# Kernel optimization log

Hardware: AMD Instinct MI355X
Metric: run time of the kernel (lower is better)

The kernel has to match this reference:

```python
import jax, jax.numpy as jnp
import numpy as np

C = 64
DQK = C // 8  # query/key channels


def setup_inputs() -> dict:
    key = jax.random.key(0)
    ks = jax.random.split(key, 8)
    B, H, W = 4, 64, 64
    x = jax.random.normal(ks[0], (B, C, H, W), dtype=jnp.float32)
    # 1x1 conv weights stored as (out_ch, in_ch); biases as (out_ch,)
    wq = jax.random.normal(ks[1], (DQK, C), dtype=jnp.float32) * 0.05
    bq = jnp.zeros((DQK,), dtype=jnp.float32)
    wk = jax.random.normal(ks[2], (DQK, C), dtype=jnp.float32) * 0.05
    bk = jnp.zeros((DQK,), dtype=jnp.float32)
    wv = jax.random.normal(ks[3], (C, C), dtype=jnp.float32) * 0.05
    bv = jnp.zeros((C,), dtype=jnp.float32)
    gamma = jnp.zeros((1,), dtype=jnp.float32)
    return {"x": x, "wq": wq, "bq": bq, "wk": wk, "bk": bk,
            "wv": wv, "bv": bv, "gamma": gamma}


def reference(x, wq, bq, wk, bk, wv, bv, gamma):
    B, Cc, H, W = x.shape
    N = H * W
    xf = x.reshape(B, Cc, N)  # (B, C, N)
    # 1x1 convs == channel-wise matmuls
    q = jnp.einsum('oc,bcn->bon', wq, xf) + bq[None, :, None]  # (B, dqk, N)
    k = jnp.einsum('oc,bcn->bon', wk, xf) + bk[None, :, None]  # (B, dqk, N)
    v = jnp.einsum('oc,bcn->bon', wv, xf) + bv[None, :, None]  # (B, C, N)
    # qk = q^T k -> (B, N, N), softmax over last dim
    qk = jnp.einsum('bdn,bdm->bnm', q, k)
    attn = jax.nn.softmax(qk, axis=-1)
    # out = v @ attn^T : out[b,c,i] = sum_j v[b,c,j] * attn[b,i,j]
    out = jnp.einsum('bcj,bij->bci', v, attn)
    out = out.reshape(B, Cc, H, W)
    return gamma * out + x
```

## Files before the change

kernel.cpp:

```cpp
#include <hip/hip_runtime.h>
#include <cmath>

namespace {

constexpr int B = 4;
constexpr int C = 64;
constexpr int N = 4096;
constexpr float LOG2E = 1.4426950408889634f;

typedef __bf16 bf16x8 __attribute__((ext_vector_type(8)));
typedef float f32x16 __attribute__((ext_vector_type(16)));
typedef unsigned short u16;

union B8 {
  int4 i;
  bf16x8 h;
  unsigned int w[4];
};

__device__ inline u16 f2bf(float f) {
  unsigned int u = __float_as_uint(f);
  u += 0x7FFFu + ((u >> 16) & 1u);
  return (u16)(u >> 16);
}

__device__ inline unsigned int cvt_pk_bf16(float lo, float hi) {
  unsigned int r;
  asm("v_cvt_pk_bf16_f32 %0, %1, %2" : "=v"(r) : "v"(lo), "v"(hi));
  return r;
}

__device__ inline float exp2_fast(float x) {
#if __has_builtin(__builtin_amdgcn_exp2f)
  return __builtin_amdgcn_exp2f(x);
#else
  return exp2f(x);
#endif
}

__device__ inline void pl32_swap(unsigned int& a, unsigned int& b) {
#if __has_builtin(__builtin_amdgcn_permlane32_swap)
  auto r = __builtin_amdgcn_permlane32_swap(a, b, false, false);
  a = (unsigned int)r[0];
  b = (unsigned int)r[1];
#else
  asm volatile("s_nop 1\n\tv_permlane32_swap_b32 %0, %1" : "+v"(a), "+v"(b));
#endif
}

__global__ __launch_bounds__(256) void qkv_kernel(
    const float* __restrict__ x,
    const float* __restrict__ wq, const float* __restrict__ bq,
    const float* __restrict__ wk, const float* __restrict__ bk,
    const float* __restrict__ wv, const float* __restrict__ bv,
    u16* __restrict__ qt, u16* __restrict__ kt, u16* __restrict__ vo) {
  const int bid = blockIdx.x;
  const int cg = bid & 3;
  const int nt = (bid >> 2) & 63;
  const int b = bid >> 8;
  const int t = threadIdx.x;
  const int nn = t & 63;
  const int wid = __builtin_amdgcn_readfirstlane(t >> 6);
  const int n = nt * 64 + nn;
  const float* xb = x + (size_t)b * C * N + n;

  const int c0 = cg * 16 + wid * 4;
  float a0 = bv[c0], a1 = bv[c0 + 1], a2 = bv[c0 + 2], a3 = bv[c0 + 3];

  if (cg == 0) {
    const int o0 = wid * 2;
    float qa0 = bq[o0], qa1 = bq[o0 + 1];
    float ka0 = bk[o0], ka1 = bk[o0 + 1];
    #pragma unroll 8
    for (int c = 0; c < C; ++c) {
      const float xv = xb[(size_t)c * N];
      a0 = fmaf(wv[(c0 + 0) * C + c], xv, a0);
      a1 = fmaf(wv[(c0 + 1) * C + c], xv, a1);
      a2 = fmaf(wv[(c0 + 2) * C + c], xv, a2);
      a3 = fmaf(wv[(c0 + 3) * C + c], xv, a3);
      qa0 = fmaf(wq[o0 * C + c], xv, qa0);
      qa1 = fmaf(wq[(o0 + 1) * C + c], xv, qa1);
      ka0 = fmaf(wk[o0 * C + c], xv, ka0);
      ka1 = fmaf(wk[(o0 + 1) * C + c], xv, ka1);
    }
    const unsigned int qw =
        (unsigned int)f2bf(qa0 * LOG2E) | ((unsigned int)f2bf(qa1 * LOG2E) << 16);
    const unsigned int kw =
        (unsigned int)f2bf(ka0) | ((unsigned int)f2bf(ka1) << 16);
    *reinterpret_cast<unsigned int*>(qt + ((size_t)b * N + n) * 8 + o0) = qw;
    *reinterpret_cast<unsigned int*>(kt + ((size_t)b * N + n) * 8 + o0) = kw;
  } else {
    #pragma unroll 8
    for (int c = 0; c < C; ++c) {
      const float xv = xb[(size_t)c * N];
      a0 = fmaf(wv[(c0 + 0) * C + c], xv, a0);
      a1 = fmaf(wv[(c0 + 1) * C + c], xv, a1);
      a2 = fmaf(wv[(c0 + 2) * C + c], xv, a2);
      a3 = fmaf(wv[(c0 + 3) * C + c], xv, a3);
    }
  }

  const size_t tb = ((size_t)b * (N / 16) + (n >> 4)) * (C * 16) + (n & 15);
  vo[tb + (size_t)(c0 + 0) * 16] = f2bf(a0);
  vo[tb + (size_t)(c0 + 1) * 16] = f2bf(a1);
  vo[tb + (size_t)(c0 + 2) * 16] = f2bf(a2);
  vo[tb + (size_t)(c0 + 3) * 16] = f2bf(a3);
}

__global__ __launch_bounds__(512, 1) void attn_kernel(
    const u16* __restrict__ qt, const u16* __restrict__ kt,
    const u16* __restrict__ vv, const float* __restrict__ x,
    const float* __restrict__ gamma, float* __restrict__ out) {
  const int b = blockIdx.x >> 6;
  const int i0 = (blockIdx.x & 63) * 64;
  const int t = threadIdx.x;
  const int lane = t & 63;
  const int w = __builtin_amdgcn_readfirstlane(t >> 6);
  const int il = lane & 31;
  const int hi = lane >> 5;

  __shared__ float l_lds[8][32];
  __shared__ u16 o_lds[8][32][66];

  B8 qf0, qf1;
  if (hi == 0) {
    qf0.i = *reinterpret_cast<const int4*>(qt + ((size_t)b * N + i0 + il) * 8);
    qf1.i = *reinterpret_cast<const int4*>(qt + ((size_t)b * N + i0 + 32 + il) * 8);
  } else {
    qf0.i = make_int4(0, 0, 0, 0);
    qf1.i = make_int4(0, 0, 0, 0);
  }

  const u16* ktb = kt + (size_t)b * N * 8;
  const u16* vbase = vv + (size_t)b * (N / 16) * (C * 16) + il * 16 + hi * 8;

  f32x16 accA0, accB0, accA1, accB1, zero16;
  #pragma unroll
  for (int r = 0; r < 16; ++r) {
    accA0[r] = 0.f; accB0[r] = 0.f; accA1[r] = 0.f; accB1[r] = 0.f;
    zero16[r] = 0.f;
  }
  float lrun0 = 0.f, lrun1 = 0.f;

  B8 kfA, va0A, va1A, vb0A, vb1A;
  B8 kfB, va0B, va1B, vb0B, vb1B;

  auto LOAD = [&](int jt, B8& kf, B8& va0, B8& va1, B8& vb0, B8& vb1) {
    const int j0 = w * 512 + jt * 32;
    if (hi == 0)
      kf.i = *reinterpret_cast<const int4*>(ktb + (size_t)(j0 + il) * 8);
    else
      kf.i = make_int4(0, 0, 0, 0);
    const u16* vp = vbase + (size_t)(j0 >> 4) * (C * 16);
    va0.i = *reinterpret_cast<const int4*>(vp);
    va1.i = *reinterpret_cast<const int4*>(vp + 1024);
    vb0.i = *reinterpret_cast<const int4*>(vp + 512);
    vb1.i = *reinterpret_cast<const int4*>(vp + 1536);
  };

  auto SMPACK = [&](const f32x16& S, float& lrun, B8& pf0, B8& pf1) {
    float p[16];
    #pragma unroll
    for (int r = 0; r < 16; ++r) p[r] = exp2_fast(S[r]);
    const float t0 = (p[0] + p[1]) + (p[2] + p[3]);
    const float t1 = (p[4] + p[5]) + (p[6] + p[7]);
    const float t2 = (p[8] + p[9]) + (p[10] + p[11]);
    const float t3 = (p[12] + p[13]) + (p[14] + p[15]);
    lrun += (t0 + t1) + (t2 + t3);
    unsigned a0 = cvt_pk_bf16(p[0], p[1]);
    unsigned a1 = cvt_pk_bf16(p[2], p[3]);
    unsigned b0 = cvt_pk_bf16(p[4], p[5]);
    unsigned b1 = cvt_pk_bf16(p[6], p[7]);
    pl32_swap(a0, b0);
    pl32_swap(a1, b1);
    pf0.w[0] = a0; pf0.w[1] = a1; pf0.w[2] = b0; pf0.w[3] = b1;
    a0 = cvt_pk_bf16(p[8], p[9]);
    a1 = cvt_pk_bf16(p[10], p[11]);
    b0 = cvt_pk_bf16(p[12], p[13]);
    b1 = cvt_pk_bf16(p[14], p[15]);
    pl32_swap(a0, b0);
    pl32_swap(a1, b1);
    pf1.w[0] = a0; pf1.w[1] = a1; pf1.w[2] = b0; pf1.w[3] = b1;
  };

  auto COMPUTE = [&](const B8& kf, const B8& va0, const B8& va1, const B8& vb0,
                     const B8& vb1) {
    f32x16 S0 = __builtin_amdgcn_mfma_f32_32x32x16_bf16(kf.h, qf0.h, zero16, 0, 0, 0);
    f32x16 S1 = __builtin_amdgcn_mfma_f32_32x32x16_bf16(kf.h, qf1.h, zero16, 0, 0, 0);
    B8 p00, p01, p10, p11;
    SMPACK(S0, lrun0, p00, p01);
    SMPACK(S1, lrun1, p10, p11);
    accA0 = __builtin_amdgcn_mfma_f32_32x32x16_bf16(va0.h, p00.h, accA0, 0, 0, 0);
    accA0 = __builtin_amdgcn_mfma_f32_32x32x16_bf16(va1.h, p01.h, accA0, 0, 0, 0);
    accB0 = __builtin_amdgcn_mfma_f32_32x32x16_bf16(vb0.h, p00.h, accB0, 0, 0, 0);
    accB0 = __builtin_amdgcn_mfma_f32_32x32x16_bf16(vb1.h, p01.h, accB0, 0, 0, 0);
    accA1 = __builtin_amdgcn_mfma_f32_32x32x16_bf16(va0.h, p10.h, accA1, 0, 0, 0);
    accA1 = __builtin_amdgcn_mfma_f32_32x32x16_bf16(va1.h, p11.h, accA1, 0, 0, 0);
    accB1 = __builtin_amdgcn_mfma_f32_32x32x16_bf16(vb0.h, p10.h, accB1, 0, 0, 0);
    accB1 = __builtin_amdgcn_mfma_f32_32x32x16_bf16(vb1.h, p11.h, accB1, 0, 0, 0);
  };

  LOAD(0, kfA, va0A, va1A, vb0A, vb1A);
  #pragma unroll 1
  for (int it = 0; it < 8; ++it) {
    LOAD(2 * it + 1, kfB, va0B, va1B, vb0B, vb1B);
    COMPUTE(kfA, va0A, va1A, vb0A, vb1A);
    if (it < 7) LOAD(2 * it + 2, kfA, va0A, va1A, vb0A, vb1A);
    COMPUTE(kfB, va0B, va1B, vb0B, vb1B);
  }

  const float lw0 = lrun0 + __shfl_xor(lrun0, 32);
  const float lw1 = lrun1 + __shfl_xor(lrun1, 32);
  const float g = gamma[0];

  #pragma unroll 2
  for (int ph = 0; ph < 2; ++ph) {
    const f32x16& aA = ph ? accA1 : accA0;
    const f32x16& aB = ph ? accB1 : accB0;
    const float lw = ph ? lw1 : lw0;
    __syncthreads();
    if (hi == 0) l_lds[w][il] = lw;
    #pragma unroll
    for (int r = 0; r < 16; r += 2) {
      const int c = (r & 3) + 8 * (r >> 2) + 4 * hi;
      *reinterpret_cast<unsigned int*>(&o_lds[w][il][c]) =
          cvt_pk_bf16(aA[r], aA[r + 1]);
      *reinterpret_cast<unsigned int*>(&o_lds[w][il][c + 32]) =
          cvt_pk_bf16(aB[r], aB[r + 1]);
    }
    __syncthreads();

    const int i = t & 31;
    float Li = 0.f;
    #pragma unroll
    for (int ww = 0; ww < 8; ++ww) Li += l_lds[ww][i];
    const float ginv = g / Li;

    #pragma unroll
    for (int q4 = 0; q4 < 4; ++q4) {
      const int flat = t + q4 * 512;
      const int c = flat >> 5;
      float s = 0.f;
      #pragma unroll
      for (int ww = 0; ww < 8; ++ww)
        s += __uint_as_float((unsigned int)o_lds[ww][i][c] << 16);
      const size_t off = ((size_t)b * C + c) * N + i0 + ph * 32 + i;
      out[off] = fmaf(ginv, s, x[off]);
    }
  }
}

}

extern "C" void kernel_launch(void* const* d_in, const int* in_sizes, int n_in,
                              void* d_out, int out_size, void* d_ws, size_t ws_size,
                              hipStream_t stream) {
  const float* x     = (const float*)d_in[0];
  const float* wq    = (const float*)d_in[1];
  const float* bq    = (const float*)d_in[2];
  const float* wk    = (const float*)d_in[3];
  const float* bk    = (const float*)d_in[4];
  const float* wv    = (const float*)d_in[5];
  const float* bv    = (const float*)d_in[6];
  const float* gamma = (const float*)d_in[7];
  float* out = (float*)d_out;

  u16* qt = (u16*)d_ws;
  u16* kt = qt + (size_t)B * N * 8;
  u16* vo = kt + (size_t)B * N * 8;

  qkv_kernel<<<B * 64 * 4, 256, 0, stream>>>(x, wq, bq, wk, bk, wv, bv, qt, kt, vo);
  attn_kernel<<<B * (N / 64), 512, 0, stream>>>(qt, kt, vo, x, gamma, out);
}
```

Baseline: 31.32 us.

## Split attention keys across 16 waves and remap blocks to XCDs by batch

The attention kernel now launches 1024 threads per block, so each of 16 waves handles 256 keys instead of 512. The two-deep prefetch of K and V is replaced by a one-tile K prefetch, with V loaded inline just before its MFMAs. The epilogue is reorganised into four phases that reduce 16 partial sums through a smaller LDS buffer. Both kernels remap block IDs so that each XCD handles one batch half, which is meant to improve L2 locality for K/V. The aim is more latency hiding through extra waves, at the cost of more cross-wave reduction work and synchronisation, and less load prefetching per wave.

```diff
diff --git a/kernel.cpp b/kernel.cpp
--- a/kernel.cpp
+++ b/kernel.cpp
@@ -55,9 +55,10 @@
     const float* __restrict__ wv, const float* __restrict__ bv,
     u16* __restrict__ qt, u16* __restrict__ kt, u16* __restrict__ vo) {
   const int bid = blockIdx.x;
-  const int cg = bid & 3;
-  const int nt = (bid >> 2) & 63;
-  const int b = bid >> 8;
+  const int xcd = bid & 7;
+  const int b = xcd >> 1;
+  const int cg = (bid >> 3) & 3;
+  const int nt = (xcd & 1) * 32 + (bid >> 5);
   const int t = threadIdx.x;
   const int nn = t & 63;
   const int wid = __builtin_amdgcn_readfirstlane(t >> 6);
@@ -107,20 +108,22 @@
   vo[tb + (size_t)(c0 + 3) * 16] = f2bf(a3);
 }
 
-__global__ __launch_bounds__(512, 1) void attn_kernel(
+__global__ __launch_bounds__(1024, 4) void attn_kernel(
     const u16* __restrict__ qt, const u16* __restrict__ kt,
     const u16* __restrict__ vv, const float* __restrict__ x,
     const float* __restrict__ gamma, float* __restrict__ out) {
-  const int b = blockIdx.x >> 6;
-  const int i0 = (blockIdx.x & 63) * 64;
+  const int bid = blockIdx.x;
+  const int xcd = bid & 7;
+  const int b = xcd >> 1;
+  const int i0 = ((xcd & 1) * 32 + (bid >> 3)) * 64;
   const int t = threadIdx.x;
   const int lane = t & 63;
   const int w = __builtin_amdgcn_readfirstlane(t >> 6);
   const int il = lane & 31;
   const int hi = lane >> 5;
 
-  __shared__ float l_lds[8][32];
-  __shared__ u16 o_lds[8][32][66];
+  __shared__ float l_lds[16][32];
+  __shared__ u16 o_lds[16][32][34];
 
   B8 qf0, qf1;
   if (hi == 0) {
@@ -131,8 +134,9 @@
     qf1.i = make_int4(0, 0, 0, 0);
   }
 
-  const u16* ktb = kt + (size_t)b * N * 8;
-  const u16* vbase = vv + (size_t)b * (N / 16) * (C * 16) + il * 16 + hi * 8;
+  const u16* kbase = kt + (size_t)b * N * 8 + ((size_t)w * 256 + il) * 8;
+  const u16* vbase = vv + (size_t)b * (N / 16) * (C * 16) +
+                     (size_t)w * 16 * (C * 16) + il * 16 + hi * 8;
 
   f32x16 accA0, accB0, accA1, accB1, zero16;
   #pragma unroll
@@ -142,20 +146,13 @@
   }
   float lrun0 = 0.f, lrun1 = 0.f;
 
-  B8 kfA, va0A, va1A, vb0A, vb1A;
-  B8 kfB, va0B, va1B, vb0B, vb1B;
-
-  auto LOAD = [&](int jt, B8& kf, B8& va0, B8& va1, B8& vb0, B8& vb1) {
-    const int j0 = w * 512 + jt * 32;
+  B8 kfA, kfB;
+
+  auto LOADK = [&](int jt, B8& kf) {
     if (hi == 0)
-      kf.i = *reinterpret_cast<const int4*>(ktb + (size_t)(j0 + il) * 8);
+      kf.i = *reinterpret_cast<const int4*>(kbase + jt * 256);
     else
       kf.i = make_int4(0, 0, 0, 0);
-    const u16* vp = vbase + (size_t)(j0 >> 4) * (C * 16);
-    va0.i = *reinterpret_cast<const int4*>(vp);
-    va1.i = *reinterpret_cast<const int4*>(vp + 1024);
-    vb0.i = *reinterpret_cast<const int4*>(vp + 512);
-    vb1.i = *reinterpret_cast<const int4*>(vp + 1536);
   };
 
   auto SMPACK = [&](const f32x16& S, float& lrun, B8& pf0, B8& pf1) {
@@ -167,86 +164,79 @@
     const float t2 = (p[8] + p[9]) + (p[10] + p[11]);
     const float t3 = (p[12] + p[13]) + (p[14] + p[15]);
     lrun += (t0 + t1) + (t2 + t3);
-    unsigned a0 = cvt_pk_bf16(p[0], p[1]);
-    unsigned a1 = cvt_pk_bf16(p[2], p[3]);
-    unsigned b0 = cvt_pk_bf16(p[4], p[5]);
-    unsigned b1 = cvt_pk_bf16(p[6], p[7]);
+    unsigned a0 = cvt_pk_bf16(p[0], p[1]), a1 = cvt_pk_bf16(p[2], p[3]);
+    unsigned b0 = cvt_pk_bf16(p[4], p[5]), b1 = cvt_pk_bf16(p[6], p[7]);
     pl32_swap(a0, b0);
     pl32_swap(a1, b1);
     pf0.w[0] = a0; pf0.w[1] = a1; pf0.w[2] = b0; pf0.w[3] = b1;
-    a0 = cvt_pk_bf16(p[8], p[9]);
-    a1 = cvt_pk_bf16(p[10], p[11]);
-    b0 = cvt_pk_bf16(p[12], p[13]);
-    b1 = cvt_pk_bf16(p[14], p[15]);
+    a0 = cvt_pk_bf16(p[8], p[9]);  a1 = cvt_pk_bf16(p[10], p[11]);
+    b0 = cvt_pk_bf16(p[12], p[13]); b1 = cvt_pk_bf16(p[14], p[15]);
     pl32_swap(a0, b0);
     pl32_swap(a1, b1);
     pf1.w[0] = a0; pf1.w[1] = a1; pf1.w[2] = b0; pf1.w[3] = b1;
   };
 
-  auto COMPUTE = [&](const B8& kf, const B8& va0, const B8& va1, const B8& vb0,
-                     const B8& vb1) {
+  auto TILE = [&](int jt, B8& kf, B8& kfn) {
     f32x16 S0 = __builtin_amdgcn_mfma_f32_32x32x16_bf16(kf.h, qf0.h, zero16, 0, 0, 0);
     f32x16 S1 = __builtin_amdgcn_mfma_f32_32x32x16_bf16(kf.h, qf1.h, zero16, 0, 0, 0);
-    B8 p00, p01, p10, p11;
-    SMPACK(S0, lrun0, p00, p01);
-    SMPACK(S1, lrun1, p10, p11);
-    accA0 = __builtin_amdgcn_mfma_f32_32x32x16_bf16(va0.h, p00.h, accA0, 0, 0, 0);
-    accA0 = __builtin_amdgcn_mfma_f32_32x32x16_bf16(va1.h, p01.h, accA0, 0, 0, 0);
-    accB0 = __builtin_amdgcn_mfma_f32_32x32x16_bf16(vb0.h, p00.h, accB0, 0, 0, 0);
-    accB0 = __builtin_amdgcn_mfma_f32_32x32x16_bf16(vb1.h, p01.h, accB0, 0, 0, 0);
-    accA1 = __builtin_amdgcn_mfma_f32_32x32x16_bf16(va0.h, p10.h, accA1, 0, 0, 0);
-    accA1 = __builtin_amdgcn_mfma_f32_32x32x16_bf16(va1.h, p11.h, accA1, 0, 0, 0);
-    accB1 = __builtin_amdgcn_mfma_f32_32x32x16_bf16(vb0.h, p10.h, accB1, 0, 0, 0);
-    accB1 = __builtin_amdgcn_mfma_f32_32x32x16_bf16(vb1.h, p11.h, accB1, 0, 0, 0);
+    if (jt + 1 < 8) LOADK(jt + 1, kfn);
+    B8 pA0, pA1, pB0, pB1;
+    SMPACK(S0, lrun0, pA0, pA1);
+    SMPACK(S1, lrun1, pB0, pB1);
+    const u16* vp = vbase + jt * 2048;
+    B8 va0, va1;
+    va0.i = *reinterpret_cast<const int4*>(vp);
+    va1.i = *reinterpret_cast<const int4*>(vp + 1024);
+    accA0 = __builtin_amdgcn_mfma_f32_32x32x16_bf16(va0.h, pA0.h, accA0, 0, 0, 0);
+    accA0 = __builtin_amdgcn_mfma_f32_32x32x16_bf16(va1.h, pA1.h, accA0, 0, 0, 0);
+    accA1 = __builtin_amdgcn_mfma_f32_32x32x16_bf16(va0.h, pB0.h, accA1, 0, 0, 0);
+    accA1 = __builtin_amdgcn_mfma_f32_32x32x16_bf16(va1.h, pB1.h, accA1, 0, 0, 0);
+    B8 vb0, vb1;
+    vb0.i = *reinterpret_cast<const int4*>(vp + 512);
+    vb1.i = *reinterpret_cast<const int4*>(vp + 1536);
+    accB0 = __builtin_amdgcn_mfma_f32_32x32x16_bf16(vb0.h, pA0.h, accB0, 0, 0, 0);
+    accB0 = __builtin_amdgcn_mfma_f32_32x32x16_bf16(vb1.h, pA1.h, accB0, 0, 0, 0);
+    accB1 = __builtin_amdgcn_mfma_f32_32x32x16_bf16(vb0.h, pB0.h, accB1, 0, 0, 0);
+    accB1 = __builtin_amdgcn_mfma_f32_32x32x16_bf16(vb1.h, pB1.h, accB1, 0, 0, 0);
   };
 
-  LOAD(0, kfA, va0A, va1A, vb0A, vb1A);
+  LOADK(0, kfA);
   #pragma unroll 1
-  for (int it = 0; it < 8; ++it) {
-    LOAD(2 * it + 1, kfB, va0B, va1B, vb0B, vb1B);
-    COMPUTE(kfA, va0A, va1A, vb0A, vb1A);
-    if (it < 7) LOAD(2 * it + 2, kfA, va0A, va1A, vb0A, vb1A);
-    COMPUTE(kfB, va0B, va1B, vb0B, vb1B);
+  for (int it = 0; it < 4; ++it) {
+    TILE(2 * it, kfA, kfB);
+    TILE(2 * it + 1, kfB, kfA);
   }
 
   const float lw0 = lrun0 + __shfl_xor(lrun0, 32);
   const float lw1 = lrun1 + __shfl_xor(lrun1, 32);
   const float g = gamma[0];
 
-  #pragma unroll 2
-  for (int ph = 0; ph < 2; ++ph) {
-    const f32x16& aA = ph ? accA1 : accA0;
-    const f32x16& aB = ph ? accB1 : accB0;
-    const float lw = ph ? lw1 : lw0;
+  #pragma unroll
+  for (int ph = 0; ph < 4; ++ph) {
+    const int qh = ph >> 1, ch = ph & 1;
+    const f32x16& acc = qh ? (ch ? accB1 : accA1) : (ch ? accB0 : accA0);
+    const float lw = qh ? lw1 : lw0;
     __syncthreads();
     if (hi == 0) l_lds[w][il] = lw;
     #pragma unroll
     for (int r = 0; r < 16; r += 2) {
       const int c = (r & 3) + 8 * (r >> 2) + 4 * hi;
       *reinterpret_cast<unsigned int*>(&o_lds[w][il][c]) =
-          cvt_pk_bf16(aA[r], aA[r + 1]);
-      *reinterpret_cast<unsigned int*>(&o_lds[w][il][c + 32]) =
-          cvt_pk_bf16(aB[r], aB[r + 1]);
+          cvt_pk_bf16(acc[r], acc[r + 1]);
     }
     __syncthreads();
 
     const int i = t & 31;
+    const int c = t >> 5;
     float Li = 0.f;
     #pragma unroll
-    for (int ww = 0; ww < 8; ++ww) Li += l_lds[ww][i];
-    const float ginv = g / Li;
-
-    #pragma unroll
-    for (int q4 = 0; q4 < 4; ++q4) {
-      const int flat = t + q4 * 512;
-      const int c = flat >> 5;
-      float s = 0.f;
-      #pragma unroll
-      for (int ww = 0; ww < 8; ++ww)
-        s += __uint_as_float((unsigned int)o_lds[ww][i][c] << 16);
-      const size_t off = ((size_t)b * C + c) * N + i0 + ph * 32 + i;
-      out[off] = fmaf(ginv, s, x[off]);
-    }
+    for (int ww = 0; ww < 16; ++ww) Li += l_lds[ww][i];
+    float s = 0.f;
+    #pragma unroll
+    for (int ww = 0; ww < 16; ++ww)
+      s += __uint_as_float((unsigned int)o_lds[ww][i][c] << 16);
+    const size_t off = ((size_t)b * C + ch * 32 + c) * N + i0 + qh * 32 + i;
+    out[off] = fmaf(g / Li, s, x[off]);
   }
 }
 
@@ -270,5 +260,5 @@
   u16* vo = kt + (size_t)B * N * 8;
 
   qkv_kernel<<<B * 64 * 4, 256, 0, stream>>>(x, wq, bq, wk, bk, wv, bv, qt, kt, vo);
-  attn_kernel<<<B * (N / 64), 512, 0, stream>>>(qt, kt, vo, x, gamma, out);
-}
+  attn_kernel<<<B * (N / 64), 1024, 0, stream>>>(qt, kt, vo, x, gamma, out);
+}
```

After: 72.54 us. +131.6%, slower.
